# Optimization experiments

Hardware: AMD Instinct MI355X
Metric: run time of the kernel (lower is better)

## Reference

```python
import jax, jax.numpy as jnp
import numpy as np

B = 32768
Z_DIM = 64
X_DIM = 256
HIDDEN = 512
T = 8            # num_transforms
NBINS = 8
TAIL = 25.0
MULT = 3 * NBINS - 1   # widths + heights + interior derivatives = 23
MIN_W = 1e-3
MIN_H = 1e-3
MIN_D = 1e-3


def _masks():
    # MADE degrees (nflows, random_mask=False)
    d_in = np.arange(1, Z_DIM + 1)                      # input degrees 1..D
    h = np.arange(HIDDEN) % (Z_DIM - 1) + 1             # hidden degrees
    o = np.arange(Z_DIM * MULT) // MULT + 1             # output degrees, MULT contiguous per feature
    m1 = (h[:, None] >= d_in[None, :]).astype(np.float32)   # [H, D]
    m2 = (h[:, None] >= h[None, :]).astype(np.float32)      # [H, H]
    m3 = (o[:, None] > h[None, :]).astype(np.float32)       # [D*MULT, H] strict for output layer
    return jnp.asarray(m1), jnp.asarray(m2), jnp.asarray(m3)


def _rq_spline_fwd(z, uw, uh, ud):
    """Unconstrained rational-quadratic spline with linear tails (forward).
    z: [B, D]; uw/uh: [B, D, NBINS]; ud: [B, D, NBINS-1].
    Returns (outputs [B,D], logabsdet [B,D])."""
    const = np.log(np.exp(1.0 - MIN_D) - 1.0)
    pad = jnp.full(ud.shape[:-1] + (1,), const, ud.dtype)
    ud = jnp.concatenate([pad, ud, pad], axis=-1)       # [B, D, NBINS+1]

    widths = jax.nn.softmax(uw, axis=-1)
    widths = MIN_W + (1.0 - MIN_W * NBINS) * widths
    zero = jnp.zeros(widths.shape[:-1] + (1,), widths.dtype)
    cumw = jnp.concatenate([zero, jnp.cumsum(widths, axis=-1)], axis=-1)
    cumw = -TAIL + 2.0 * TAIL * cumw
    cumw = cumw.at[..., 0].set(-TAIL).at[..., -1].set(TAIL)
    widths = cumw[..., 1:] - cumw[..., :-1]

    derivs = MIN_D + jax.nn.softplus(ud)

    heights = jax.nn.softmax(uh, axis=-1)
    heights = MIN_H + (1.0 - MIN_H * NBINS) * heights
    cumh = jnp.concatenate([zero, jnp.cumsum(heights, axis=-1)], axis=-1)
    cumh = -TAIL + 2.0 * TAIL * cumh
    cumh = cumh.at[..., 0].set(-TAIL).at[..., -1].set(TAIL)
    heights = cumh[..., 1:] - cumh[..., :-1]

    delta = heights / widths

    z_in = jnp.clip(z, -TAIL, TAIL)
    edges = cumw.at[..., -1].add(1e-6)                  # nflows searchsorted eps
    idx = jnp.sum(z_in[..., None] >= edges, axis=-1) - 1
    idx = jnp.clip(idx, 0, NBINS - 1)

    g = lambda a: jnp.take_along_axis(a, idx[..., None], axis=-1)[..., 0]
    in_cw = g(cumw); in_w = g(widths)
    in_ch = g(cumh); in_h = g(heights)
    in_dl = g(delta)
    d0 = g(derivs); d1 = g(derivs[..., 1:])

    th = (z_in - in_cw) / in_w
    th1 = th * (1.0 - th)
    num = in_h * (in_dl * th * th + d0 * th1)
    den = in_dl + (d0 + d1 - 2.0 * in_dl) * th1
    out = in_ch + num / den
    dnum = in_dl ** 2 * (d1 * th * th + 2.0 * in_dl * th1 + d0 * (1.0 - th) ** 2)
    lad = jnp.log(dnum) - 2.0 * jnp.log(den)

    inside = (z >= -TAIL) & (z <= TAIL)
    return jnp.where(inside, out, z), jnp.where(inside, lad, 0.0)


def setup_inputs() -> dict:
    key = jax.random.key(0)
    ks = jax.random.split(key, 10)
    s = 0.05  # small init scale keeps spline params in a sane regime
    return {
        "z": jax.random.normal(ks[0], (B, Z_DIM), jnp.float32),
        "x": jax.random.normal(ks[1], (B, X_DIM), jnp.float32),
        "W1": jax.random.normal(ks[2], (T, HIDDEN, Z_DIM), jnp.float32) * s,
        "b1": jax.random.normal(ks[3], (T, HIDDEN), jnp.float32) * s,
        "Wc": jax.random.normal(ks[4], (T, HIDDEN, X_DIM), jnp.float32) * s,
        "bc": jax.random.normal(ks[5], (T, HIDDEN), jnp.float32) * s,
        "W2": jax.random.normal(ks[6], (T, HIDDEN, HIDDEN), jnp.float32) * s,
        "b2": jax.random.normal(ks[7], (T, HIDDEN), jnp.float32) * s,
        "W3": jax.random.normal(ks[8], (T, Z_DIM * MULT, HIDDEN), jnp.float32) * s,
        "b3": jax.random.normal(ks[9], (T, Z_DIM * MULT), jnp.float32) * s,
    }


def reference(z, x, W1, b1, Wc, bc, W2, b2, W3, b3):
    """log q(z|x) of the composed MADE-RQ-spline flow, shape [B]."""
    m1, m2, m3 = _masks()
    inv_sqrt_h = 1.0 / np.sqrt(HIDDEN)
    cur = z
    total_lad = jnp.zeros(z.shape[0], z.dtype)
    for t in range(T):
        # MADE: masked initial layer + context layer, one masked feedforward block (linear->relu), masked output layer
        h = cur @ (W1[t] * m1).T + b1[t] + x @ Wc[t].T + bc[t]
        h = jax.nn.relu(h @ (W2[t] * m2).T + b2[t])
        p = (h @ (W3[t] * m3).T + b3[t]).reshape(-1, Z_DIM, MULT)
        uw = p[..., :NBINS] * inv_sqrt_h
        uh = p[..., NBINS:2 * NBINS] * inv_sqrt_h
        ud = p[..., 2 * NBINS:]
        cur, lad = _rq_spline_fwd(cur, uw, uh, ud)
        total_lad = total_lad + lad.sum(axis=-1)
    log_base = -0.5 * jnp.sum(cur ** 2, axis=-1) - 0.5 * Z_DIM * np.log(2.0 * np.pi)
    return log_base + total_lad
```

## Files before the change

kernel.cpp:

```cpp
#include <hip/hip_runtime.h>
#include <cstdint>
#include <cstddef>

#define B_ROWS 32768
#define ZD 64
#define XD 256
#define HID 512
#define T_STEPS 8
#define MULT 23
#define MPAD 24
#define NOUT 1472
#define NPAD 1536
#define K1 320
#define PSTRIDE 200

typedef float f32x4 __attribute__((ext_vector_type(4)));
typedef short s16x8 __attribute__((ext_vector_type(8)));

__device__ __forceinline__ unsigned short f2bf(float f) {
  unsigned int u = __float_as_uint(f);
  u = (u + 0x7FFFu + ((u >> 16) & 1u)) >> 16;
  return (unsigned short)u;
}
__device__ __forceinline__ float bf2f(unsigned short s) {
  return __uint_as_float(((unsigned int)s) << 16);
}

__device__ __forceinline__ int permP(int n) {
  return (n < 72) ? (n / 9) + 63 * (n % 9)
                  : ((n - 72) >> 3) + 8 + 63 * ((n - 72) & 7);
}
__device__ __forceinline__ int degP(int n) {
  return (n < 72) ? (n / 9) + 1 : ((n - 72) >> 3) + 9;
}


__global__ void prep_weights(const float* __restrict__ W1, const float* __restrict__ Wc,
                             const float* __restrict__ W2, const float* __restrict__ W3,
                             const float* __restrict__ b1, const float* __restrict__ bc,
                             const float* __restrict__ b2, const float* __restrict__ b3,
                             unsigned short* __restrict__ w1c, unsigned short* __restrict__ w2c,
                             unsigned short* __restrict__ w3c,
                             float* __restrict__ ob1, float* __restrict__ ob2,
                             float* __restrict__ ob3) {
  const int S1 = T_STEPS * HID * K1;
  const int S2 = S1 + T_STEPS * HID * HID;
  const int S3 = S2 + T_STEPS * NPAD * HID;
  const int S4 = S3 + T_STEPS * HID;
  const int S5 = S4 + T_STEPS * HID;
  const int S6 = S5 + T_STEPS * NPAD;
  int i = blockIdx.x * 256 + threadIdx.x;
  if (i < S1) {
    int t = i / (HID * K1);
    int r = i - t * (HID * K1);
    int n = r / K1;
    int k = r - n * K1;
    int on = permP(n);
    float v;
    if (k < ZD) v = ((on % 63) >= k) ? W1[((size_t)t * HID + on) * ZD + k] : 0.0f;
    else        v = Wc[((size_t)t * HID + on) * XD + (k - ZD)];
    w1c[i] = f2bf(v);
  } else if (i < S2) {
    int j = i - S1;
    int t = j / (HID * HID);
    int r = j - t * (HID * HID);
    int n = r / HID;
    int k = r - n * HID;
    float v = 0.0f;
    if (degP(n) >= degP(k))
      v = W2[((size_t)t * HID + permP(n)) * HID + permP(k)];
    w2c[j] = f2bf(v);
  } else if (i < S3) {
    int j = i - S2;
    int t = j / (NPAD * HID);
    int r = j - t * (NPAD * HID);
    int n = r / HID;
    int k = r - n * HID;
    int d = n / MPAD;
    int jj = n - d * MPAD;
    float v = 0.0f;
    if (jj < MULT && d >= degP(k))
      v = W3[((size_t)t * NOUT + d * MULT + jj) * HID + permP(k)];
    w3c[j] = f2bf(v);
  } else if (i < S4) {
    int j = i - S3;
    int t = j / HID, n = j - t * HID;
    int on = permP(n);
    ob1[j] = b1[(size_t)t * HID + on] + bc[(size_t)t * HID + on];
  } else if (i < S5) {
    int j = i - S4;
    int t = j / HID, n = j - t * HID;
    ob2[j] = b2[(size_t)t * HID + permP(n)];
  } else if (i < S6) {
    int j = i - S5;
    int t = j / NPAD;
    int n = j - t * NPAD;
    int d = n / MPAD;
    int jj = n - d * MPAD;
    ob3[j] = (jj < MULT) ? b3[(size_t)t * NOUT + d * MULT + jj] : 0.0f;
  }
}

__global__ void prep_data(const float* __restrict__ x, const float* __restrict__ z,
                          unsigned short* __restrict__ A1,
                          float* __restrict__ curf, float* __restrict__ out) {
  const int SX = B_ROWS * XD;
  int i = blockIdx.x * 256 + threadIdx.x;
  if (i < SX) {
    int b = i >> 8;
    int j = i & 255;
    A1[(size_t)b * K1 + ZD + j] = f2bf(x[i]);
  } else {
    int j = i - SX;
    if (j < B_ROWS * ZD) {
      int b = j >> 6;
      int d = j & 63;
      float zv = z[j];
      A1[(size_t)b * K1 + d] = f2bf(zv);
      curf[j] = zv;
      if (d == 0) out[b] = -58.81206612509905f;
    }
  }
}


#define ASYNC16(gp, lp) __builtin_amdgcn_global_load_lds( \
    (__attribute__((address_space(1))) unsigned int*)(gp), \
    (__attribute__((address_space(3))) unsigned int*)(lp), 16, 0, 0)

#define WAITV(n) asm volatile("s_waitcnt vmcnt(" #n ")" ::: "memory")


__global__ __launch_bounds__(256, 3) void gemm_bias(
    const unsigned short* __restrict__ A,
    const unsigned short* __restrict__ Bw,
    const float* __restrict__ bias,
    unsigned short* __restrict__ C,
    int M, int N, int K, int relu, int tri)
{
  __shared__ alignas(16) unsigned short lS[3][8192];

  const int tid  = threadIdx.x;
  const int lane = tid & 63;
  const int wave = tid >> 6;

  const int lin = blockIdx.y * 4 + blockIdx.x;
  const int xcd = lin & 7;
  const int loc = lin >> 3;
  const int m0 = (xcd * 32 + (loc >> 2)) * 128;
  const int n0 = (loc & 3) * 128;
  const int Keff = tri ? min(K, 192 + n0) : K;
  const int nIter = Keff >> 5;

  const int wm = (wave >> 1) * 64;
  const int wn = (wave & 1) * 64;

  const int f    = tid * 16;
  const int row0 = f >> 6;
  const int colb = f & 63;

  char* gA0 = (char*)A  + ((size_t)(m0 + row0) * K) * 2 + colb;
  char* gA1 = gA0 + (size_t)64 * K * 2;
  char* gB0 = (char*)Bw + ((size_t)(n0 + row0) * K) * 2 + colb;
  char* gB1 = gB0 + (size_t)64 * K * 2;

  f32x4 acc[4][4];
#pragma unroll
  for (int i = 0; i < 4; i++)
#pragma unroll
    for (int j = 0; j < 4; j++) acc[i][j] = (f32x4){0.f, 0.f, 0.f, 0.f};

  const int fr = lane & 15;
  const int fk = (lane >> 4) * 8;

#define STAGEB(sp) do { \
    unsigned short* s_ = (sp) + wave * 512; \
    ASYNC16(gA0, s_); \
    ASYNC16(gA1, s_ + 2048); \
    ASYNC16(gB0, s_ + 4096); \
    ASYNC16(gB1, s_ + 6144); \
    gA0 += 64; gA1 += 64; gB0 += 64; gB1 += 64; \
  } while (0)

  STAGEB(lS[0]);
  STAGEB(lS[1]);

  for (int k = 0; k < nIter; ++k) {
    __builtin_amdgcn_sched_barrier(0);
    if (k + 2 < nIter) STAGEB(lS[0] + ((k + 2) % 3) * 8192);
    const int nv = nIter - 1 - k;
    if (nv >= 2)      WAITV(8);
    else if (nv == 1) WAITV(4);
    else              WAITV(0);
    __builtin_amdgcn_s_barrier();
    __builtin_amdgcn_sched_barrier(0);

    const unsigned short* cs = lS[0] + (k % 3) * 8192;
    s16x8 a[4], b[4];
#pragma unroll
    for (int i = 0; i < 4; i++)
      a[i] = *(const s16x8*)(cs + (wm + i * 16 + fr) * 32 + fk);
#pragma unroll
    for (int j = 0; j < 4; j++)
      b[j] = *(const s16x8*)(cs + 4096 + (wn + j * 16 + fr) * 32 + fk);

#pragma unroll
    for (int i = 0; i < 4; i++)
#pragma unroll
      for (int j = 0; j < 4; j++)
        acc[i][j] = __builtin_amdgcn_mfma_f32_16x16x32_bf16(a[i], b[j], acc[i][j], 0, 0, 0);

    __builtin_amdgcn_sched_barrier(0);
    __builtin_amdgcn_s_barrier();
  }
#undef STAGEB

#pragma unroll
  for (int j = 0; j < 4; j++) {
    const int col = n0 + wn + j * 16 + fr;
    const float bv = bias[col];
#pragma unroll
    for (int i = 0; i < 4; i++) {
      const int rbase = m0 + wm + i * 16 + (lane >> 4) * 4;
#pragma unroll
      for (int r = 0; r < 4; r++) {
        float v = acc[i][j][r] + bv;
        if (relu) v = fmaxf(v, 0.0f);
        C[(size_t)(rbase + r) * N + col] = f2bf(v);
      }
    }
  }
}


__device__ __forceinline__ void rq_spline(const unsigned short* __restrict__ pp,
                                          float zv, float& zn, float& lad) {
  const float TAILC = 25.0f;
  const float MIN_WC = 0.001f;
  const float MIN_DC = 0.001f;
  const float SCALE2 = 0.06376007120095582f;
  const float LN2 = 0.6931471805599453f;

  s16x8 vw = *(const s16x8*)(pp);
  s16x8 vh = *(const s16x8*)(pp + 8);
  s16x8 vd = *(const s16x8*)(pp + 16);

  bool inside = (zv >= -TAILC) && (zv <= TAILC);
  float z_in = fminf(fmaxf(zv, -TAILC), TAILC);

  float ew[8], eh[8], sw = 0.f, sh = 0.f;
#pragma unroll
  for (int i = 0; i < 8; i++) {
    ew[i] = exp2f(bf2f((unsigned short)vw[i]) * SCALE2); sw += ew[i];
  }
#pragma unroll
  for (int i = 0; i < 8; i++) {
    eh[i] = exp2f(bf2f((unsigned short)vh[i]) * SCALE2); sh += eh[i];
  }
  float iw = (1.0f - 8.0f * MIN_WC) / sw;
  float ih = (1.0f - 8.0f * MIN_WC) / sh;

  float cumw[9], cumh[9];
  cumw[0] = -TAILC; cumh[0] = -TAILC;
  float cw = 0.f, ch = 0.f;
#pragma unroll
  for (int i = 0; i < 8; i++) {
    cw += MIN_WC + ew[i] * iw;
    ch += MIN_WC + eh[i] * ih;
    cumw[i + 1] = fmaf(2.0f * TAILC, cw, -TAILC);
    cumh[i + 1] = fmaf(2.0f * TAILC, ch, -TAILC);
  }
  cumw[8] = TAILC; cumh[8] = TAILC;

  int idx = 0;
#pragma unroll
  for (int i = 1; i < 8; i++) idx += (z_in >= cumw[i]) ? 1 : 0;

  float in_cw = 0.f, cw1 = 1.f, in_ch = 0.f, ch1 = 1.f, u0 = 0.f, u1 = 0.f;
#pragma unroll
  for (int i = 0; i < 8; i++) {
    if (i == idx) {
      in_cw = cumw[i]; cw1 = cumw[i + 1];
      in_ch = cumh[i]; ch1 = cumh[i + 1];
      u0 = (i > 0) ? bf2f((unsigned short)vd[i - 1]) : 0.0f;
      u1 = (i < 7) ? bf2f((unsigned short)vd[i]) : 0.0f;
    }
  }
  float dd0 = (idx == 0) ? 1.0f
            : MIN_DC + fmaxf(u0, 0.f) + __logf(1.0f + __expf(-fabsf(u0)));
  float dd1 = (idx == 7) ? 1.0f
            : MIN_DC + fmaxf(u1, 0.f) + __logf(1.0f + __expf(-fabsf(u1)));
  float in_w = cw1 - in_cw;
  float in_h = ch1 - in_ch;

  float delta = in_h / in_w;
  float th  = (z_in - in_cw) / in_w;
  float th1 = th * (1.0f - th);
  float th2 = th * th;
  float num = in_h * (delta * th2 + dd0 * th1);
  float den = delta + (dd0 + dd1 - 2.0f * delta) * th1;
  float outz = in_ch + num / den;
  float omt = 1.0f - th;
  float dnum = delta * delta * (dd1 * th2 + 2.0f * delta * th1 + dd0 * omt * omt);
  float l = LN2 * (__log2f(dnum) - 2.0f * __log2f(den));

  zn  = inside ? outz : zv;
  lad = inside ? l : 0.0f;
}


__global__ __launch_bounds__(256, 3) void gemm3_spline(
    const unsigned short* __restrict__ A,
    const unsigned short* __restrict__ Bw,
    const float* __restrict__ bias,
    float* __restrict__ curf,
    unsigned short* __restrict__ A1,
    float* __restrict__ out,
    int last)
{
  __shared__ alignas(16) union {
    struct { unsigned short A[2 * 128 * 32]; unsigned short B[2 * 192 * 32]; } g;
    unsigned short p[64 * PSTRIDE];
  } sm;

  const int tid  = threadIdx.x;
  const int lane = tid & 63;
  const int wave = tid >> 6;

  const int lin = blockIdx.y * 8 + blockIdx.x;
  const int xcd = lin & 7;
  const int loc = lin >> 3;
  const int m0 = (xcd * 32 + (loc >> 3)) * 128;
  const int bn = loc & 7;
  const int n0 = bn * 192;
  const int Keff = 64 * (bn + 1);

  const int wm = (wave >> 1) * 64;
  const int wn = (wave & 1) * 96;
  const int fr = lane & 15;
  const int fk = (lane >> 4) * 8;

  const int srow64 = tid & 63;
  const int dloc  = wave * 2;
  const int dglob = bn * 8 + dloc;
  const size_t czoff0 = (size_t)(m0 + srow64) * ZD + dglob;
  const size_t czoff1 = (size_t)(m0 + 64 + srow64) * ZD + dglob;
  float2 cz0 = *(const float2*)(curf + czoff0);
  float2 cz1 = *(const float2*)(curf + czoff1);
  float bv[6];
#pragma unroll
  for (int j = 0; j < 6; j++) bv[j] = bias[n0 + wn + j * 16 + fr];

  const int f    = tid * 16;
  const int row0 = f >> 6;
  const int colb = f & 63;
  const int K = HID;

  char* gA0 = (char*)A  + ((size_t)(m0 + row0) * K) * 2 + colb;
  char* gA1 = gA0 + (size_t)64 * K * 2;
  char* gB0 = (char*)Bw + ((size_t)(n0 + row0) * K) * 2 + colb;
  char* gB1 = gB0 + (size_t)64 * K * 2;
  char* gB2 = gB1 + (size_t)64 * K * 2;

  unsigned short* lA0 = sm.g.A + wave * 512;
  unsigned short* lA1 = sm.g.A + 2048 + wave * 512;
  unsigned short* lB0 = sm.g.B + wave * 512;
  unsigned short* lB1 = sm.g.B + 2048 + wave * 512;
  unsigned short* lB2 = sm.g.B + 4096 + wave * 512;

  f32x4 acc[4][6];
#pragma unroll
  for (int i = 0; i < 4; i++)
#pragma unroll
    for (int j = 0; j < 6; j++) acc[i][j] = (f32x4){0.f, 0.f, 0.f, 0.f};

  for (int k0 = 0; k0 < Keff; k0 += 64) {
    ASYNC16(gA0, lA0);
    ASYNC16(gA1, lA1);
    ASYNC16(gB0, lB0);
    ASYNC16(gB1, lB1);
    ASYNC16(gB2, lB2);
    ASYNC16(gA0 + 64, lA0 + 4096);
    ASYNC16(gA1 + 64, lA1 + 4096);
    ASYNC16(gB0 + 64, lB0 + 6144);
    ASYNC16(gB1 + 64, lB1 + 6144);
    ASYNC16(gB2 + 64, lB2 + 6144);
    gA0 += 128; gA1 += 128; gB0 += 128; gB1 += 128; gB2 += 128;
    __syncthreads();

    s16x8 a0[4], a1[4], b0[6], b1[6];
#pragma unroll
    for (int i = 0; i < 4; i++) {
      a0[i] = *(const s16x8*)(sm.g.A + (wm + i * 16 + fr) * 32 + fk);
      a1[i] = *(const s16x8*)(sm.g.A + 4096 + (wm + i * 16 + fr) * 32 + fk);
    }
#pragma unroll
    for (int j = 0; j < 6; j++) {
      b0[j] = *(const s16x8*)(sm.g.B + (wn + j * 16 + fr) * 32 + fk);
      b1[j] = *(const s16x8*)(sm.g.B + 6144 + (wn + j * 16 + fr) * 32 + fk);
    }

#pragma unroll
    for (int i = 0; i < 4; i++)
#pragma unroll
      for (int j = 0; j < 6; j++)
        acc[i][j] = __builtin_amdgcn_mfma_f32_16x16x32_bf16(a0[i], b0[j], acc[i][j], 0, 0, 0);
#pragma unroll
    for (int i = 0; i < 4; i++)
#pragma unroll
      for (int j = 0; j < 6; j++)
        acc[i][j] = __builtin_amdgcn_mfma_f32_16x16x32_bf16(a1[i], b1[j], acc[i][j], 0, 0, 0);
    __syncthreads();
  }

#pragma unroll
  for (int h = 0; h < 2; ++h) {
    if ((wave >> 1) == h) {
#pragma unroll
      for (int j = 0; j < 6; j++) {
        const int col = wn + j * 16 + fr;
#pragma unroll
        for (int i = 0; i < 4; i++) {
          const int rloc = i * 16 + (lane >> 4) * 4;
#pragma unroll
          for (int r = 0; r < 4; r++)
            sm.p[(rloc + r) * PSTRIDE + col] = f2bf(acc[i][j][r] + bv[j]);
        }
      }
    }
    __syncthreads();

    {
      const int sbr = m0 + h * 64 + srow64;
      const float2 czv = h ? cz1 : cz0;
      const unsigned short* pp = sm.p + srow64 * PSTRIDE + dloc * MPAD;
      float zn0, zn1, l0, l1;
      rq_spline(pp,        czv.x, zn0, l0);
      rq_spline(pp + MPAD, czv.y, zn1, l1);

      *(float2*)(curf + (size_t)sbr * ZD + dglob) = make_float2(zn0, zn1);
      unsigned int pkv = (unsigned int)f2bf(zn0) | ((unsigned int)f2bf(zn1) << 16);
      *(unsigned int*)(A1 + (size_t)sbr * K1 + dglob) = pkv;

      float contrib = l0 + l1;
      if (last) contrib -= 0.5f * (zn0 * zn0 + zn1 * zn1);
      atomicAdd(&out[sbr], contrib);
    }
    if (h == 0) __syncthreads();
  }
}


extern "C" void kernel_launch(void* const* d_in, const int* in_sizes, int n_in,
                              void* d_out, int out_size, void* d_ws, size_t ws_size,
                              hipStream_t stream)
{
  const float* z  = (const float*)d_in[0];
  const float* x  = (const float*)d_in[1];
  const float* W1 = (const float*)d_in[2];
  const float* b1 = (const float*)d_in[3];
  const float* Wc = (const float*)d_in[4];
  const float* bc = (const float*)d_in[5];
  const float* W2 = (const float*)d_in[6];
  const float* b2 = (const float*)d_in[7];
  const float* W3 = (const float*)d_in[8];
  const float* b3 = (const float*)d_in[9];
  float* out = (float*)d_out;
  char* ws = (char*)d_ws;

  size_t oA1 = 0;
  size_t oH1 = oA1 + (size_t)B_ROWS * K1 * 2;
  size_t oH2 = oH1 + (size_t)B_ROWS * HID * 2;
  size_t oCU = oH2 + (size_t)B_ROWS * HID * 2;
  size_t oW1 = oCU + (size_t)B_ROWS * ZD * 4;
  size_t oW2 = oW1 + (size_t)T_STEPS * HID * K1 * 2;
  size_t oW3 = oW2 + (size_t)T_STEPS * HID * HID * 2;
  size_t oB1 = oW3 + (size_t)T_STEPS * NPAD * HID * 2;
  size_t oB2 = oB1 + (size_t)T_STEPS * HID * 4;
  size_t oB3 = oB2 + (size_t)T_STEPS * HID * 4;

  unsigned short* A1  = (unsigned short*)(ws + oA1);
  unsigned short* h1  = (unsigned short*)(ws + oH1);
  unsigned short* h2  = (unsigned short*)(ws + oH2);
  float* curf = (float*)(ws + oCU);
  unsigned short* w1c = (unsigned short*)(ws + oW1);
  unsigned short* w2c = (unsigned short*)(ws + oW2);
  unsigned short* w3c = (unsigned short*)(ws + oW3);
  float* b1c = (float*)(ws + oB1);
  float* b2p = (float*)(ws + oB2);
  float* b3c = (float*)(ws + oB3);

  const int prepw_total = T_STEPS * (HID * K1 + HID * HID + NPAD * HID + 2 * HID + NPAD);
  prep_weights<<<(prepw_total + 255) / 256, 256, 0, stream>>>(
      W1, Wc, W2, W3, b1, bc, b2, b3, w1c, w2c, w3c, b1c, b2p, b3c);
  const int prepd_total = B_ROWS * (XD + ZD);
  prep_data<<<(prepd_total + 255) / 256, 256, 0, stream>>>(x, z, A1, curf, out);

  for (int t = 0; t < T_STEPS; ++t) {
    gemm_bias<<<dim3(4, B_ROWS / 128), 256, 0, stream>>>(
        A1, w1c + (size_t)t * HID * K1, b1c + (size_t)t * HID, h1,
        B_ROWS, HID, K1, 0, 0);
    gemm_bias<<<dim3(4, B_ROWS / 128), 256, 0, stream>>>(
        h1, w2c + (size_t)t * HID * HID, b2p + (size_t)t * HID, h2,
        B_ROWS, HID, HID, 1, 1);
    gemm3_spline<<<dim3(8, B_ROWS / 128), 256, 0, stream>>>(
        h2, w3c + (size_t)t * NPAD * HID, b3c + (size_t)t * NPAD,
        curf, A1, out, (t == T_STEPS - 1) ? 1 : 0);
  }
}
```

Baseline: 1.007 ms.

## Keep full A row tile resident in LDS and loop over all N blocks per workgroup

```diff
diff --git a/kernel.cpp b/kernel.cpp
--- a/kernel.cpp
+++ b/kernel.cpp
@@ -13,6 +13,7 @@
 #define NPAD 1536
 #define K1 320
 #define PSTRIDE 200
+#define ASTRIDE 520
 
 typedef float f32x4 __attribute__((ext_vector_type(4)));
 typedef short s16x8 __attribute__((ext_vector_type(8)));
@@ -309,7 +310,7 @@
 }
 
 
-__global__ __launch_bounds__(256, 3) void gemm3_spline(
+__global__ __launch_bounds__(256, 1) void gemm3_spline(
     const unsigned short* __restrict__ A,
     const unsigned short* __restrict__ Bw,
     const float* __restrict__ bias,
@@ -318,22 +319,25 @@
     float* __restrict__ out,
     int last)
 {
+  __shared__ alignas(16) unsigned short Ac[128 * ASTRIDE];
   __shared__ alignas(16) union {
-    struct { unsigned short A[2 * 128 * 32]; unsigned short B[2 * 192 * 32]; } g;
+    unsigned short B[2 * 192 * 32];
     unsigned short p[64 * PSTRIDE];
   } sm;
 
   const int tid  = threadIdx.x;
   const int lane = tid & 63;
   const int wave = tid >> 6;
-
-  const int lin = blockIdx.y * 8 + blockIdx.x;
-  const int xcd = lin & 7;
-  const int loc = lin >> 3;
-  const int m0 = (xcd * 32 + (loc >> 3)) * 128;
-  const int bn = loc & 7;
-  const int n0 = bn * 192;
-  const int Keff = 64 * (bn + 1);
+  const int m0   = blockIdx.x * 128;
+
+  {
+    const char* gA = (const char*)A + ((size_t)m0 << 10) + lane * 16;
+#pragma unroll
+    for (int s = 0; s < 32; ++s) {
+      const int row = wave + s * 4;
+      ASYNC16(gA + ((size_t)row << 10), (char*)Ac + row * (ASTRIDE * 2));
+    }
+  }
 
   const int wm = (wave >> 1) * 64;
   const int wn = (wave & 1) * 96;
@@ -341,113 +345,112 @@
   const int fk = (lane >> 4) * 8;
 
   const int srow64 = tid & 63;
-  const int dloc  = wave * 2;
-  const int dglob = bn * 8 + dloc;
-  const size_t czoff0 = (size_t)(m0 + srow64) * ZD + dglob;
-  const size_t czoff1 = (size_t)(m0 + 64 + srow64) * ZD + dglob;
-  float2 cz0 = *(const float2*)(curf + czoff0);
-  float2 cz1 = *(const float2*)(curf + czoff1);
-  float bv[6];
-#pragma unroll
-  for (int j = 0; j < 6; j++) bv[j] = bias[n0 + wn + j * 16 + fr];
+  const int dloc   = wave * 2;
 
   const int f    = tid * 16;
   const int row0 = f >> 6;
   const int colb = f & 63;
-  const int K = HID;
-
-  char* gA0 = (char*)A  + ((size_t)(m0 + row0) * K) * 2 + colb;
-  char* gA1 = gA0 + (size_t)64 * K * 2;
-  char* gB0 = (char*)Bw + ((size_t)(n0 + row0) * K) * 2 + colb;
-  char* gB1 = gB0 + (size_t)64 * K * 2;
-  char* gB2 = gB1 + (size_t)64 * K * 2;
-
-  unsigned short* lA0 = sm.g.A + wave * 512;
-  unsigned short* lA1 = sm.g.A + 2048 + wave * 512;
-  unsigned short* lB0 = sm.g.B + wave * 512;
-  unsigned short* lB1 = sm.g.B + 2048 + wave * 512;
-  unsigned short* lB2 = sm.g.B + 4096 + wave * 512;
-
-  f32x4 acc[4][6];
-#pragma unroll
-  for (int i = 0; i < 4; i++)
-#pragma unroll
-    for (int j = 0; j < 6; j++) acc[i][j] = (f32x4){0.f, 0.f, 0.f, 0.f};
-
-  for (int k0 = 0; k0 < Keff; k0 += 64) {
-    ASYNC16(gA0, lA0);
-    ASYNC16(gA1, lA1);
-    ASYNC16(gB0, lB0);
-    ASYNC16(gB1, lB1);
-    ASYNC16(gB2, lB2);
-    ASYNC16(gA0 + 64, lA0 + 4096);
-    ASYNC16(gA1 + 64, lA1 + 4096);
-    ASYNC16(gB0 + 64, lB0 + 6144);
-    ASYNC16(gB1 + 64, lB1 + 6144);
-    ASYNC16(gB2 + 64, lB2 + 6144);
-    gA0 += 128; gA1 += 128; gB0 += 128; gB1 += 128; gB2 += 128;
-    __syncthreads();
-
-    s16x8 a0[4], a1[4], b0[6], b1[6];
-#pragma unroll
-    for (int i = 0; i < 4; i++) {
-      a0[i] = *(const s16x8*)(sm.g.A + (wm + i * 16 + fr) * 32 + fk);
-      a1[i] = *(const s16x8*)(sm.g.A + 4096 + (wm + i * 16 + fr) * 32 + fk);
+
+  float la0 = 0.f, la1 = 0.f;
+
+  for (int bn = 0; bn < 8; ++bn) {
+    const int n0 = bn * 192;
+    const int dglob = bn * 8 + dloc;
+    float2 cz0 = *(const float2*)(curf + (size_t)(m0 + srow64) * ZD + dglob);
+    float2 cz1 = *(const float2*)(curf + (size_t)(m0 + 64 + srow64) * ZD + dglob);
+    float bv[6];
+#pragma unroll
+    for (int j = 0; j < 6; j++) bv[j] = bias[n0 + wn + j * 16 + fr];
+
+    char* gB0 = (char*)Bw + (((size_t)(n0 + row0)) << 10) + colb;
+    char* gB1 = gB0 + ((size_t)64 << 10);
+    char* gB2 = gB1 + ((size_t)64 << 10);
+    unsigned short* lB0 = sm.B + wave * 512;
+    unsigned short* lB1 = sm.B + 2048 + wave * 512;
+    unsigned short* lB2 = sm.B + 4096 + wave * 512;
+
+    f32x4 acc[4][6];
+#pragma unroll
+    for (int i = 0; i < 4; i++)
+#pragma unroll
+      for (int j = 0; j < 6; j++) acc[i][j] = (f32x4){0.f, 0.f, 0.f, 0.f};
+
+    const int Keff = 64 * (bn + 1);
+    for (int k0 = 0; k0 < Keff; k0 += 64) {
+      ASYNC16(gB0, lB0);
+      ASYNC16(gB1, lB1);
+      ASYNC16(gB2, lB2);
+      ASYNC16(gB0 + 64, lB0 + 6144);
+      ASYNC16(gB1 + 64, lB1 + 6144);
+      ASYNC16(gB2 + 64, lB2 + 6144);
+      gB0 += 128; gB1 += 128; gB2 += 128;
+      __syncthreads();
+
+      s16x8 a0[4], a1[4], b0[6], b1[6];
+#pragma unroll
+      for (int i = 0; i < 4; i++) {
+        const unsigned short* ar = Ac + (wm + i * 16 + fr) * ASTRIDE + k0 + fk;
+        a0[i] = *(const s16x8*)(ar);
+        a1[i] = *(const s16x8*)(ar + 32);
+      }
+#pragma unroll
+      for (int j = 0; j < 6; j++) {
+        b0[j] = *(const s16x8*)(sm.B + (wn + j * 16 + fr) * 32 + fk);
+        b1[j] = *(const s16x8*)(sm.B + 6144 + (wn + j * 16 + fr) * 32 + fk);
+      }
+
+#pragma unroll
+      for (int i = 0; i < 4; i++)
+#pragma unroll
+        for (int j = 0; j < 6; j++)
+          acc[i][j] = __builtin_amdgcn_mfma_f32_16x16x32_bf16(a0[i], b0[j], acc[i][j], 0, 0, 0);
+#pragma unroll
+      for (int i = 0; i < 4; i++)
+#pragma unroll
+        for (int j = 0; j < 6; j++)
+          acc[i][j] = __builtin_amdgcn_mfma_f32_16x16x32_bf16(a1[i], b1[j], acc[i][j], 0, 0, 0);
+      __syncthreads();
     }
-#pragma unroll
-    for (int j = 0; j < 6; j++) {
-      b0[j] = *(const s16x8*)(sm.g.B + (wn + j * 16 + fr) * 32 + fk);
-      b1[j] = *(const s16x8*)(sm.g.B + 6144 + (wn + j * 16 + fr) * 32 + fk);
-    }
-
-#pragma unroll
-    for (int i = 0; i < 4; i++)
-#pragma unroll
-      for (int j = 0; j < 6; j++)
-        acc[i][j] = __builtin_amdgcn_mfma_f32_16x16x32_bf16(a0[i], b0[j], acc[i][j], 0, 0, 0);
-#pragma unroll
-    for (int i = 0; i < 4; i++)
-#pragma unroll
-      for (int j = 0; j < 6; j++)
-        acc[i][j] = __builtin_amdgcn_mfma_f32_16x16x32_bf16(a1[i], b1[j], acc[i][j], 0, 0, 0);
-    __syncthreads();
-  }
-
-#pragma unroll
-  for (int h = 0; h < 2; ++h) {
-    if ((wave >> 1) == h) {
-#pragma unroll
-      for (int j = 0; j < 6; j++) {
-        const int col = wn + j * 16 + fr;
-#pragma unroll
-        for (int i = 0; i < 4; i++) {
-          const int rloc = i * 16 + (lane >> 4) * 4;
-#pragma unroll
-          for (int r = 0; r < 4; r++)
-            sm.p[(rloc + r) * PSTRIDE + col] = f2bf(acc[i][j][r] + bv[j]);
+
+#pragma unroll
+    for (int h = 0; h < 2; ++h) {
+      if ((wave >> 1) == h) {
+#pragma unroll
+        for (int j = 0; j < 6; j++) {
+          const int col = wn + j * 16 + fr;
+#pragma unroll
+          for (int i = 0; i < 4; i++) {
+            const int rloc = i * 16 + (lane >> 4) * 4;
+#pragma unroll
+            for (int r = 0; r < 4; r++)
+              sm.p[(rloc + r) * PSTRIDE + col] = f2bf(acc[i][j][r] + bv[j]);
+          }
         }
       }
+      __syncthreads();
+
+      {
+        const int sbr = m0 + h * 64 + srow64;
+        const float2 czv = h ? cz1 : cz0;
+        const unsigned short* pp = sm.p + srow64 * PSTRIDE + dloc * MPAD;
+        float zn0, zn1, l0, l1;
+        rq_spline(pp,        czv.x, zn0, l0);
+        rq_spline(pp + MPAD, czv.y, zn1, l1);
+
+        *(float2*)(curf + (size_t)sbr * ZD + dglob) = make_float2(zn0, zn1);
+        unsigned int pkv = (unsigned int)f2bf(zn0) | ((unsigned int)f2bf(zn1) << 16);
+        *(unsigned int*)(A1 + (size_t)sbr * K1 + dglob) = pkv;
+
+        float c = l0 + l1;
+        if (last) c -= 0.5f * (zn0 * zn0 + zn1 * zn1);
+        if (h == 0) la0 += c; else la1 += c;
+      }
+      __syncthreads();
     }
-    __syncthreads();
-
-    {
-      const int sbr = m0 + h * 64 + srow64;
-      const float2 czv = h ? cz1 : cz0;
-      const unsigned short* pp = sm.p + srow64 * PSTRIDE + dloc * MPAD;
-      float zn0, zn1, l0, l1;
-      rq_spline(pp,        czv.x, zn0, l0);
-      rq_spline(pp + MPAD, czv.y, zn1, l1);
-
-      *(float2*)(curf + (size_t)sbr * ZD + dglob) = make_float2(zn0, zn1);
-      unsigned int pkv = (unsigned int)f2bf(zn0) | ((unsigned int)f2bf(zn1) << 16);
-      *(unsigned int*)(A1 + (size_t)sbr * K1 + dglob) = pkv;
-
-      float contrib = l0 + l1;
-      if (last) contrib -= 0.5f * (zn0 * zn0 + zn1 * zn1);
-      atomicAdd(&out[sbr], contrib);
-    }
-    if (h == 0) __syncthreads();
-  }
+  }
+
+  atomicAdd(&out[m0 + srow64], la0);
+  atomicAdd(&out[m0 + 64 + srow64], la1);
 }
 
 
@@ -503,7 +506,7 @@
     gemm_bias<<<dim3(4, B_ROWS / 128), 256, 0, stream>>>(
         h1, w2c + (size_t)t * HID * HID, b2p + (size_t)t * HID, h2,
         B_ROWS, HID, HID, 1, 1);
-    gemm3_spline<<<dim3(8, B_ROWS / 128), 256, 0, stream>>>(
+    gemm3_spline<<<dim3(B_ROWS / 128), 256, 0, stream>>>(
         h2, w3c + (size_t)t * NPAD * HID, b3c + (size_t)t * NPAD,
         curf, A1, out, (t == T_STEPS - 1) ? 1 : 0);
   }
```

New measurement: 1.349 ms. 34.0% more time.
